# Kernel optimization log

Measured on AMD Instinct MI355X. Metric: run time of the kernel, lower is better.

Reference implementation:

```python
import jax, jax.numpy as jnp
import numpy as np

N_NODES = 50000
IN_DIM = 128
OUT_DIM = 128
N_EDGES = 800000


def setup_inputs() -> dict:
    key = jax.random.key(0)
    k1, k2, k3, k4 = jax.random.split(key, 4)
    h = jax.random.normal(k1, (N_NODES, IN_DIM), dtype=jnp.float32)
    edges = jax.random.randint(k2, (2, N_EDGES), 0, N_NODES, dtype=jnp.int64)
    # nn.Linear params
    lim = 1.0 / np.sqrt(IN_DIM)
    W = jax.random.uniform(k3, (OUT_DIM, IN_DIM), minval=-lim, maxval=lim, dtype=jnp.float32)
    b = jax.random.uniform(k4, (OUT_DIM,), minval=-lim, maxval=lim, dtype=jnp.float32)
    return {"h": h, "W": W, "b": b, "edges": edges}


def reference(h, W, b, edges):
    n = h.shape[0]
    # add self loops (use_self_loops=True)
    loops = jnp.arange(n, dtype=edges.dtype)
    src = jnp.concatenate([edges[0], loops])  # [E+N]
    dst = jnp.concatenate([edges[1], loops])  # [E+N]
    # linear transform
    h_ = h @ W.T + b  # [N, out_dim]
    # symmetric normalization: 1/sqrt(deg(src)*deg(dst)), degrees incl. self loops
    deg = jax.ops.segment_sum(jnp.ones_like(dst, dtype=h.dtype), dst, num_segments=n)
    ew = jax.lax.rsqrt(deg[src] * deg[dst])  # [E+N]
    # edge-weighted scatter-sum aggregation
    agg = jax.ops.segment_sum(h_[src] * ew[:, None], dst, num_segments=n)
    return agg
```

## Files before the change

kernel.cpp:

```cpp
#include <hip/hip_runtime.h>


#define IN_DIM 128
#define OUT_DIM 128
#define CAP 40
#define NB_A 256
#define NBIN 196
#define BINW 256
#define CAPA 44
#define OVB 8
#define OVCAP 4096

typedef short bf16x8 __attribute__((ext_vector_type(8)));
typedef float f32x4 __attribute__((ext_vector_type(4)));
typedef unsigned short us8 __attribute__((ext_vector_type(8)));
typedef unsigned short us4 __attribute__((ext_vector_type(4)));

__device__ __forceinline__ unsigned short f2bf(float f) {
    unsigned u = __float_as_uint(f);
    u += 0x7fffu + ((u >> 16) & 1u);
    return (unsigned short)(u >> 16);
}
__device__ __forceinline__ float bf2f(unsigned short s) {
    return __uint_as_float(((unsigned)s) << 16);
}
__device__ __forceinline__ void accw(float4& acc, ushort4 v, float wt) {
    acc.x += wt * bf2f(v.x);
    acc.y += wt * bf2f(v.y);
    acc.z += wt * bf2f(v.z);
    acc.w += wt * bf2f(v.w);
}
__device__ __forceinline__ bf16x8 load_a8(const float* h, int row, int k0, int n) {
    bf16x8 r;
    if (row < n) {
        const float4* p = (const float4*)(h + (size_t)row * 128 + k0);
        float4 f0 = p[0], f1 = p[1];
        r[0] = (short)f2bf(f0.x); r[1] = (short)f2bf(f0.y);
        r[2] = (short)f2bf(f0.z); r[3] = (short)f2bf(f0.w);
        r[4] = (short)f2bf(f1.x); r[5] = (short)f2bf(f1.y);
        r[6] = (short)f2bf(f1.z); r[7] = (short)f2bf(f1.w);
    } else {
        r = (bf16x8){0, 0, 0, 0, 0, 0, 0, 0};
    }
    return r;
}

__global__ __launch_bounds__(256) void k_gb(
        const float* __restrict__ h, const float* __restrict__ W,
        const float* __restrict__ b, unsigned short* __restrict__ hsb, int n,
        const int* __restrict__ ed, unsigned* __restrict__ gbuf,
        int* __restrict__ gcnt, int* __restrict__ aovb, int2* __restrict__ aov,
        int* __restrict__ ctrs, int E, int ngemm) {
    __shared__ __align__(16) unsigned short sB[128 * 136];
    __shared__ int ovc;
    __shared__ int2 ovl[OVB];
    const int tid = threadIdx.x;

    if ((int)blockIdx.x >= ngemm) {
        int blk = blockIdx.x - ngemm;
        if (blk == 0 && tid == 0) ctrs[0] = 0;
        int* bc = (int*)sB;
        for (int i = tid; i < NBIN; i += 256) bc[i] = 0;
        if (tid == 0) ovc = 0;
        __syncthreads();
        const int chunk = (E + NB_A - 1) / NB_A;
        const int e0 = blk * chunk, e1 = min(E, e0 + chunk);
        for (int e = e0 + tid; e < e1; e += 256) {
            int s = ed[e];
            int d = ed[E + e];
            int bin = d >> 8, dlo = d & 255;
            int r = atomicAdd(&bc[bin], 1);
            if (r < CAPA) {
                gbuf[((size_t)blk * NBIN + bin) * CAPA + r] =
                    (unsigned)s | ((unsigned)dlo << 16);
            } else {
                int k = atomicAdd(&ovc, 1);
                if (k < OVB) ovl[k] = make_int2(s, d);
            }
        }
        __syncthreads();
        for (int i = tid; i < NBIN; i += 256)
            gcnt[(size_t)blk * NBIN + i] = min(bc[i], CAPA);
        int nov = min(ovc, OVB);
        if (tid < nov) aov[blk * OVB + tid] = ovl[tid];
        if (tid == 0) aovb[blk] = nov;
        return;
    }

    const int lane = tid & 63;
    const int wv = tid >> 6;
    const int quad = lane >> 4;
    const int l16 = lane & 15;
    const int row0 = blockIdx.x * 128;

    {
        const float4* W4 = (const float4*)W;
        for (int t = tid; t < 128 * 32; t += 256) {
            float4 w = W4[t];
            ushort4 q;
            q.x = f2bf(w.x); q.y = f2bf(w.y); q.z = f2bf(w.z); q.w = f2bf(w.w);
            ((ushort4*)sB)[(t >> 5) * 34 + (t & 31)] = q;
        }
    }
    __syncthreads();

    f32x4 acc[2][8];
#pragma unroll
    for (int mt = 0; mt < 2; ++mt)
#pragma unroll
        for (int nt = 0; nt < 8; ++nt) acc[mt][nt] = (f32x4){0.f, 0.f, 0.f, 0.f};

    const int koff = quad * 8;
    const int ra0 = row0 + wv * 32 + l16;
    const int ra1 = ra0 + 16;
#pragma unroll
    for (int kc = 0; kc < 4; ++kc) {
        int kbase = kc * 32 + koff;
        bf16x8 a0 = load_a8(h, ra0, kbase, n);
        bf16x8 a1 = load_a8(h, ra1, kbase, n);
#pragma unroll
        for (int nt = 0; nt < 8; ++nt) {
            bf16x8 bb = *(const bf16x8*)(sB + (nt * 16 + l16) * 136 + kbase);
            acc[0][nt] = __builtin_amdgcn_mfma_f32_16x16x32_bf16(a0, bb, acc[0][nt], 0, 0, 0);
            acc[1][nt] = __builtin_amdgcn_mfma_f32_16x16x32_bf16(a1, bb, acc[1][nt], 0, 0, 0);
        }
    }

#pragma unroll
    for (int mt = 0; mt < 2; ++mt) {
#pragma unroll
        for (int r = 0; r < 4; ++r) {
            int row = row0 + wv * 32 + mt * 16 + quad * 4 + r;
            if (row >= n) continue;
#pragma unroll
            for (int nt = 0; nt < 8; ++nt) {
                int col = nt * 16 + l16;
                hsb[(size_t)row * 128 + col] = f2bf(acc[mt][nt][r] + b[col]);
            }
        }
    }
}

__global__ __launch_bounds__(256) void k_binB(const unsigned* __restrict__ gbuf,
                                              const int* __restrict__ gcnt,
                                              const int* __restrict__ aovb,
                                              const int2* __restrict__ aov,
                                              unsigned short* __restrict__ ell,
                                              int* __restrict__ cnt,
                                              float* __restrict__ rs,
                                              int2* __restrict__ ovf2,
                                              int* __restrict__ ovf2c, int n) {
    __shared__ int pfx[NB_A + 1];
    __shared__ int ws4[4];
    __shared__ int lcnt[BINW];
    __shared__ __align__(16) unsigned short ells[BINW * CAP];
    const int tid = threadIdx.x;
    const int bin = blockIdx.x;
    const int node0 = bin << 8;
    const int lane = tid & 63;
    const int wv = tid >> 6;

    lcnt[tid] = 0;
    int c = gcnt[(size_t)tid * NBIN + bin];
    int x = c;
#pragma unroll
    for (int d = 1; d < 64; d <<= 1) {
        int t = __shfl_up(x, d, 64);
        if (lane >= d) x += t;
    }
    if (lane == 63) ws4[wv] = x;
    __syncthreads();
    if (tid == 0) {
        int a = 0;
#pragma unroll
        for (int j = 0; j < 4; ++j) { int t = ws4[j]; ws4[j] = a; a += t; }
    }
    __syncthreads();
    pfx[tid + 1] = ws4[wv] + x;
    if (tid == 0) pfx[0] = 0;
    __syncthreads();
    const int total = pfx[NB_A];

    for (int base = 0; base < total; base += 256) {
        int idx = base + tid;
        if (idx < total) {
            int lo = 0, hi = NB_A;
            while (hi - lo > 1) {
                int mid = (lo + hi) >> 1;
                if (pfx[mid] <= idx) lo = mid; else hi = mid;
            }
            unsigned rec = gbuf[((size_t)lo * NBIN + bin) * CAPA + (idx - pfx[lo])];
            int src = rec & 0xffff;
            int dlo = rec >> 16;
            int r = atomicAdd(&lcnt[dlo], 1);
            if (r < CAP) {
                ells[dlo * CAP + r] = (unsigned short)src;
            } else {
                int k = atomicAdd(ovf2c, 1);
                if (k < OVCAP) ovf2[k] = make_int2(src, node0 + dlo);
            }
        }
    }
    {
        int cov = aovb[tid];
        for (int j = 0; j < cov; ++j) {
            int2 p = aov[tid * OVB + j];
            if ((p.y >> 8) == bin) {
                int dlo = p.y & 255;
                int r = atomicAdd(&lcnt[dlo], 1);
                if (r < CAP) {
                    ells[dlo * CAP + r] = (unsigned short)p.x;
                } else {
                    int k = atomicAdd(ovf2c, 1);
                    if (k < OVCAP) ovf2[k] = make_int2(p.x, node0 + dlo);
                }
            }
        }
    }
    __syncthreads();
    int node = node0 + tid;
    if (node < n) {
        cnt[node] = lcnt[tid];
        rs[node] = rsqrtf((float)(lcnt[tid] + 1));
    }
    const int4* sp = (const int4*)ells;
    int4* dp = (int4*)(ell + (size_t)node0 * CAP);
#pragma unroll
    for (int i = tid; i < BINW * CAP * 2 / 16; i += 256) dp[i] = sp[i];
}

__global__ __launch_bounds__(256) void k_agg(const int* __restrict__ cnt,
                                             const float* __restrict__ rs,
                                             const unsigned short* __restrict__ ell,
                                             const int2* __restrict__ ovf2,
                                             const int* __restrict__ ovf2c,
                                             const unsigned short* __restrict__ hsb,
                                             float* __restrict__ out, int n) {
    int node = blockIdx.x * 8 + (threadIdx.x >> 5);
    if (node >= n) return;
    int lane = threadIdx.x & 31;
    int deg = cnt[node];
    float rsn = rs[node];
    int m = min(deg, CAP);

    const ushort4* hp = (const ushort4*)hsb;
    ushort4 sv = hp[(size_t)node * 32 + lane];
    float4 acc;
    acc.x = rsn * bf2f(sv.x); acc.y = rsn * bf2f(sv.y);
    acc.z = rsn * bf2f(sv.z); acc.w = rsn * bf2f(sv.w);

    const unsigned short* row = ell + (size_t)node * CAP;
    int e = 0;
    for (; e + 8 <= m; e += 8) {
        us8 p = *(const us8*)(row + e);
        float w0 = rs[p[0]], w1 = rs[p[1]], w2 = rs[p[2]], w3 = rs[p[3]];
        float w4 = rs[p[4]], w5 = rs[p[5]], w6 = rs[p[6]], w7 = rs[p[7]];
        ushort4 v0 = hp[(size_t)p[0] * 32 + lane];
        ushort4 v1 = hp[(size_t)p[1] * 32 + lane];
        ushort4 v2 = hp[(size_t)p[2] * 32 + lane];
        ushort4 v3 = hp[(size_t)p[3] * 32 + lane];
        ushort4 v4 = hp[(size_t)p[4] * 32 + lane];
        ushort4 v5 = hp[(size_t)p[5] * 32 + lane];
        ushort4 v6 = hp[(size_t)p[6] * 32 + lane];
        ushort4 v7 = hp[(size_t)p[7] * 32 + lane];
        accw(acc, v0, w0); accw(acc, v1, w1); accw(acc, v2, w2); accw(acc, v3, w3);
        accw(acc, v4, w4); accw(acc, v5, w5); accw(acc, v6, w6); accw(acc, v7, w7);
    }
    if (e + 4 <= m) {
        us4 p = *(const us4*)(row + e);
        float w0 = rs[p[0]], w1 = rs[p[1]], w2 = rs[p[2]], w3 = rs[p[3]];
        ushort4 v0 = hp[(size_t)p[0] * 32 + lane];
        ushort4 v1 = hp[(size_t)p[1] * 32 + lane];
        ushort4 v2 = hp[(size_t)p[2] * 32 + lane];
        ushort4 v3 = hp[(size_t)p[3] * 32 + lane];
        accw(acc, v0, w0); accw(acc, v1, w1); accw(acc, v2, w2); accw(acc, v3, w3);
        e += 4;
    }
    for (; e < m; ++e) {
        int s = row[e];
        accw(acc, hp[(size_t)s * 32 + lane], rs[s]);
    }
    if (deg > CAP) {
        int novf = min(*ovf2c, OVCAP);
        for (int i = 0; i < novf; ++i) {
            int2 p = ovf2[i];
            if (p.y == node) {
                accw(acc, hp[(size_t)p.x * 32 + lane], rs[p.x]);
            }
        }
    }
    acc.x *= rsn; acc.y *= rsn; acc.z *= rsn; acc.w *= rsn;
    ((float4*)out)[(size_t)node * 32 + lane] = acc;
}

extern "C" void kernel_launch(void* const* d_in, const int* in_sizes, int n_in,
                              void* d_out, int out_size, void* d_ws, size_t ws_size,
                              hipStream_t stream) {
    const float* h = (const float*)d_in[0];
    const float* W = (const float*)d_in[1];
    const float* b = (const float*)d_in[2];
    const int* edges = (const int*)d_in[3];

    const int n = in_sizes[0] / IN_DIM;
    const int E = in_sizes[3] / 2;
    const int ngemm = (n + 127) / 128;
    const int nnode_pad = NBIN * BINW;

    size_t o = 0;
    auto carve = [&](size_t elems) {
        size_t cur = o;
        o += (elems + 511) & ~(size_t)511;
        return cur;
    };
    float* ws = (float*)d_ws;
    unsigned short* hsb = (unsigned short*)(ws + carve((size_t)n * 64));
    unsigned* gbuf = (unsigned*)(ws + carve((size_t)NB_A * NBIN * CAPA));
    int* gcnt = (int*)(ws + carve((size_t)NB_A * NBIN));
    int* aovb = (int*)(ws + carve(NB_A));
    int2* aov = (int2*)(ws + carve((size_t)NB_A * OVB * 2));
    int* cnt = (int*)(ws + carve(nnode_pad));
    float* rs = ws + carve(nnode_pad);
    unsigned short* ell = (unsigned short*)(ws + carve((size_t)nnode_pad * CAP / 2));
    int2* ovf2 = (int2*)(ws + carve(OVCAP * 2));
    int* ctrs = (int*)(ws + carve(2));

    float* out = (float*)d_out;

    k_gb<<<ngemm + NB_A, 256, 0, stream>>>(h, W, b, hsb, n, edges, gbuf, gcnt,
                                           aovb, aov, ctrs, E, ngemm);
    k_binB<<<NBIN, 256, 0, stream>>>(gbuf, gcnt, aovb, aov, ell, cnt, rs,
                                     ovf2, ctrs, n);
    k_agg<<<(n + 7) / 8, 256, 0, stream>>>(cnt, rs, ell, ovf2, ctrs, hsb, out, n);
}
```

Baseline: 143.5 us.

## Use finer destination bins and 16-lane 16-byte gathers in aggregation

Destination bins shrink from 256 to 64 nodes, giving 784 bins with a 16-record capacity per producer block. This lets each thread in the bin kernel scan one producer cell directly, replacing the block prefix scan and the per-record binary search. The aggregation kernel now gives each node 16 lanes that each load 8 bf16 values at once, so every gathered row is fetched with wider loads and each block covers twice as many nodes. The cost is more bin blocks, uneven per-thread serial loops in the bin kernel, and more register pressure in aggregation from the 8-float accumulators.

Result: no change. 142.6 us (-0.6%).

```diff
diff --git a/kernel.cpp b/kernel.cpp
--- a/kernel.cpp
+++ b/kernel.cpp
@@ -5,9 +5,9 @@
 #define OUT_DIM 128
 #define CAP 40
 #define NB_A 256
-#define NBIN 196
-#define BINW 256
-#define CAPA 44
+#define NBIN 784
+#define BINW 64
+#define CAPA 16
 #define OVB 8
 #define OVCAP 4096
 
@@ -23,12 +23,6 @@
 }
 __device__ __forceinline__ float bf2f(unsigned short s) {
     return __uint_as_float(((unsigned)s) << 16);
-}
-__device__ __forceinline__ void accw(float4& acc, ushort4 v, float wt) {
-    acc.x += wt * bf2f(v.x);
-    acc.y += wt * bf2f(v.y);
-    acc.z += wt * bf2f(v.z);
-    acc.w += wt * bf2f(v.w);
 }
 __device__ __forceinline__ bf16x8 load_a8(const float* h, int row, int k0, int n) {
     bf16x8 r;
@@ -68,7 +62,7 @@
         for (int e = e0 + tid; e < e1; e += 256) {
             int s = ed[e];
             int d = ed[E + e];
-            int bin = d >> 8, dlo = d & 255;
+            int bin = d >> 6, dlo = d & 63;
             int r = atomicAdd(&bc[bin], 1);
             if (r < CAPA) {
                 gbuf[((size_t)blk * NBIN + bin) * CAPA + r] =
@@ -150,46 +144,20 @@
                                               float* __restrict__ rs,
                                               int2* __restrict__ ovf2,
                                               int* __restrict__ ovf2c, int n) {
-    __shared__ int pfx[NB_A + 1];
-    __shared__ int ws4[4];
     __shared__ int lcnt[BINW];
     __shared__ __align__(16) unsigned short ells[BINW * CAP];
     const int tid = threadIdx.x;
     const int bin = blockIdx.x;
-    const int node0 = bin << 8;
-    const int lane = tid & 63;
-    const int wv = tid >> 6;
-
-    lcnt[tid] = 0;
-    int c = gcnt[(size_t)tid * NBIN + bin];
-    int x = c;
-#pragma unroll
-    for (int d = 1; d < 64; d <<= 1) {
-        int t = __shfl_up(x, d, 64);
-        if (lane >= d) x += t;
-    }
-    if (lane == 63) ws4[wv] = x;
+    const int node0 = bin * BINW;
+
+    if (tid < BINW) lcnt[tid] = 0;
     __syncthreads();
-    if (tid == 0) {
-        int a = 0;
-#pragma unroll
-        for (int j = 0; j < 4; ++j) { int t = ws4[j]; ws4[j] = a; a += t; }
-    }
-    __syncthreads();
-    pfx[tid + 1] = ws4[wv] + x;
-    if (tid == 0) pfx[0] = 0;
-    __syncthreads();
-    const int total = pfx[NB_A];
-
-    for (int base = 0; base < total; base += 256) {
-        int idx = base + tid;
-        if (idx < total) {
-            int lo = 0, hi = NB_A;
-            while (hi - lo > 1) {
-                int mid = (lo + hi) >> 1;
-                if (pfx[mid] <= idx) lo = mid; else hi = mid;
-            }
-            unsigned rec = gbuf[((size_t)lo * NBIN + bin) * CAPA + (idx - pfx[lo])];
+
+    {
+        int c = gcnt[(size_t)tid * NBIN + bin];
+        const unsigned* cell = gbuf + ((size_t)tid * NBIN + bin) * CAPA;
+        for (int j = 0; j < c; ++j) {
+            unsigned rec = cell[j];
             int src = rec & 0xffff;
             int dlo = rec >> 16;
             int r = atomicAdd(&lcnt[dlo], 1);
@@ -205,8 +173,8 @@
         int cov = aovb[tid];
         for (int j = 0; j < cov; ++j) {
             int2 p = aov[tid * OVB + j];
-            if ((p.y >> 8) == bin) {
-                int dlo = p.y & 255;
+            if ((p.y >> 6) == bin) {
+                int dlo = p.y & 63;
                 int r = atomicAdd(&lcnt[dlo], 1);
                 if (r < CAP) {
                     ells[dlo * CAP + r] = (unsigned short)p.x;
@@ -218,10 +186,12 @@
         }
     }
     __syncthreads();
-    int node = node0 + tid;
-    if (node < n) {
-        cnt[node] = lcnt[tid];
-        rs[node] = rsqrtf((float)(lcnt[tid] + 1));
+    if (tid < BINW) {
+        int node = node0 + tid;
+        if (node < n) {
+            cnt[node] = lcnt[tid];
+            rs[node] = rsqrtf((float)(lcnt[tid] + 1));
+        }
     }
     const int4* sp = (const int4*)ells;
     int4* dp = (int4*)(ell + (size_t)node0 * CAP);
@@ -236,18 +206,18 @@
                                              const int* __restrict__ ovf2c,
                                              const unsigned short* __restrict__ hsb,
                                              float* __restrict__ out, int n) {
-    int node = blockIdx.x * 8 + (threadIdx.x >> 5);
+    int node = blockIdx.x * 16 + (threadIdx.x >> 4);
     if (node >= n) return;
-    int lane = threadIdx.x & 31;
+    int lane = threadIdx.x & 15;
     int deg = cnt[node];
     float rsn = rs[node];
     int m = min(deg, CAP);
 
-    const ushort4* hp = (const ushort4*)hsb;
-    ushort4 sv = hp[(size_t)node * 32 + lane];
-    float4 acc;
-    acc.x = rsn * bf2f(sv.x); acc.y = rsn * bf2f(sv.y);
-    acc.z = rsn * bf2f(sv.z); acc.w = rsn * bf2f(sv.w);
+    const us8* hp = (const us8*)hsb;
+    us8 sv = hp[(size_t)node * 16 + lane];
+    float acc[8];
+#pragma unroll
+    for (int k = 0; k < 8; ++k) acc[k] = rsn * bf2f((unsigned short)sv[k]);
 
     const unsigned short* row = ell + (size_t)node * CAP;
     int e = 0;
@@ -255,42 +225,66 @@
         us8 p = *(const us8*)(row + e);
         float w0 = rs[p[0]], w1 = rs[p[1]], w2 = rs[p[2]], w3 = rs[p[3]];
         float w4 = rs[p[4]], w5 = rs[p[5]], w6 = rs[p[6]], w7 = rs[p[7]];
-        ushort4 v0 = hp[(size_t)p[0] * 32 + lane];
-        ushort4 v1 = hp[(size_t)p[1] * 32 + lane];
-        ushort4 v2 = hp[(size_t)p[2] * 32 + lane];
-        ushort4 v3 = hp[(size_t)p[3] * 32 + lane];
-        ushort4 v4 = hp[(size_t)p[4] * 32 + lane];
-        ushort4 v5 = hp[(size_t)p[5] * 32 + lane];
-        ushort4 v6 = hp[(size_t)p[6] * 32 + lane];
-        ushort4 v7 = hp[(size_t)p[7] * 32 + lane];
-        accw(acc, v0, w0); accw(acc, v1, w1); accw(acc, v2, w2); accw(acc, v3, w3);
-        accw(acc, v4, w4); accw(acc, v5, w5); accw(acc, v6, w6); accw(acc, v7, w7);
+        us8 v0 = hp[(size_t)p[0] * 16 + lane];
+        us8 v1 = hp[(size_t)p[1] * 16 + lane];
+        us8 v2 = hp[(size_t)p[2] * 16 + lane];
+        us8 v3 = hp[(size_t)p[3] * 16 + lane];
+        us8 v4 = hp[(size_t)p[4] * 16 + lane];
+        us8 v5 = hp[(size_t)p[5] * 16 + lane];
+        us8 v6 = hp[(size_t)p[6] * 16 + lane];
+        us8 v7 = hp[(size_t)p[7] * 16 + lane];
+#pragma unroll
+        for (int k = 0; k < 8; ++k) {
+            acc[k] += w0 * bf2f((unsigned short)v0[k]);
+            acc[k] += w1 * bf2f((unsigned short)v1[k]);
+            acc[k] += w2 * bf2f((unsigned short)v2[k]);
+            acc[k] += w3 * bf2f((unsigned short)v3[k]);
+            acc[k] += w4 * bf2f((unsigned short)v4[k]);
+            acc[k] += w5 * bf2f((unsigned short)v5[k]);
+            acc[k] += w6 * bf2f((unsigned short)v6[k]);
+            acc[k] += w7 * bf2f((unsigned short)v7[k]);
+        }
     }
     if (e + 4 <= m) {
         us4 p = *(const us4*)(row + e);
         float w0 = rs[p[0]], w1 = rs[p[1]], w2 = rs[p[2]], w3 = rs[p[3]];
-        ushort4 v0 = hp[(size_t)p[0] * 32 + lane];
-        ushort4 v1 = hp[(size_t)p[1] * 32 + lane];
-        ushort4 v2 = hp[(size_t)p[2] * 32 + lane];
-        ushort4 v3 = hp[(size_t)p[3] * 32 + lane];
-        accw(acc, v0, w0); accw(acc, v1, w1); accw(acc, v2, w2); accw(acc, v3, w3);
+        us8 v0 = hp[(size_t)p[0] * 16 + lane];
+        us8 v1 = hp[(size_t)p[1] * 16 + lane];
+        us8 v2 = hp[(size_t)p[2] * 16 + lane];
+        us8 v3 = hp[(size_t)p[3] * 16 + lane];
+#pragma unroll
+        for (int k = 0; k < 8; ++k) {
+            acc[k] += w0 * bf2f((unsigned short)v0[k]);
+            acc[k] += w1 * bf2f((unsigned short)v1[k]);
+            acc[k] += w2 * bf2f((unsigned short)v2[k]);
+            acc[k] += w3 * bf2f((unsigned short)v3[k]);
+        }
         e += 4;
     }
     for (; e < m; ++e) {
         int s = row[e];
-        accw(acc, hp[(size_t)s * 32 + lane], rs[s]);
+        float wt = rs[s];
+        us8 v = hp[(size_t)s * 16 + lane];
+#pragma unroll
+        for (int k = 0; k < 8; ++k) acc[k] += wt * bf2f((unsigned short)v[k]);
     }
     if (deg > CAP) {
         int novf = min(*ovf2c, OVCAP);
         for (int i = 0; i < novf; ++i) {
             int2 p = ovf2[i];
             if (p.y == node) {
-                accw(acc, hp[(size_t)p.x * 32 + lane], rs[p.x]);
-            }
-        }
-    }
-    acc.x *= rsn; acc.y *= rsn; acc.z *= rsn; acc.w *= rsn;
-    ((float4*)out)[(size_t)node * 32 + lane] = acc;
+                float wt = rs[p.x];
+                us8 v = hp[(size_t)p.x * 16 + lane];
+#pragma unroll
+                for (int k = 0; k < 8; ++k) acc[k] += wt * bf2f((unsigned short)v[k]);
+            }
+        }
+    }
+    float4 o0 = make_float4(rsn * acc[0], rsn * acc[1], rsn * acc[2], rsn * acc[3]);
+    float4 o1 = make_float4(rsn * acc[4], rsn * acc[5], rsn * acc[6], rsn * acc[7]);
+    float* op = out + (size_t)node * 128 + lane * 8;
+    *(float4*)op = o0;
+    *(float4*)(op + 4) = o1;
 }
 
 extern "C" void kernel_launch(void* const* d_in, const int* in_sizes, int n_in,
@@ -330,5 +324,5 @@
                                            aovb, aov, ctrs, E, ngemm);
     k_binB<<<NBIN, 256, 0, stream>>>(gbuf, gcnt, aovb, aov, ell, cnt, rs,
                                      ovf2, ctrs, n);
-    k_agg<<<(n + 7) / 8, 256, 0, stream>>>(cnt, rs, ell, ovf2, ctrs, hsb, out, n);
-}
+    k_agg<<<(n + 15) / 16, 256, 0, stream>>>(cnt, rs, ell, ovf2, ctrs, hsb, out, n);
+}
```

## Use finer 64-node destination bins and per-thread cell walks in binning

Applied to the files above, without the earlier changes.

Destination bins shrink from 256 to 64 nodes, so there are 784 bins with a per-block cell capacity of 16. The second binning kernel now launches four times as many blocks. Each thread walks its own source-block cell instead of the block building a prefix scan and doing a binary search. This removes the scan, the extra syncs and the search, and gives more parallelism in the second pass. The cost is more serial per-thread loops, more bin counters and gcnt entries, and a higher chance of overflow with the smaller CAPA of 16.

Measured after the change: 140.4 us. 1.02x faster.

```diff
diff --git a/kernel.cpp b/kernel.cpp
--- a/kernel.cpp
+++ b/kernel.cpp
@@ -5,9 +5,9 @@
 #define OUT_DIM 128
 #define CAP 40
 #define NB_A 256
-#define NBIN 196
-#define BINW 256
-#define CAPA 44
+#define NBIN 784
+#define BINW 64
+#define CAPA 16
 #define OVB 8
 #define OVCAP 4096
 
@@ -68,7 +68,7 @@
         for (int e = e0 + tid; e < e1; e += 256) {
             int s = ed[e];
             int d = ed[E + e];
-            int bin = d >> 8, dlo = d & 255;
+            int bin = d >> 6, dlo = d & 63;
             int r = atomicAdd(&bc[bin], 1);
             if (r < CAPA) {
                 gbuf[((size_t)blk * NBIN + bin) * CAPA + r] =
@@ -150,46 +150,20 @@
                                               float* __restrict__ rs,
                                               int2* __restrict__ ovf2,
                                               int* __restrict__ ovf2c, int n) {
-    __shared__ int pfx[NB_A + 1];
-    __shared__ int ws4[4];
     __shared__ int lcnt[BINW];
     __shared__ __align__(16) unsigned short ells[BINW * CAP];
     const int tid = threadIdx.x;
     const int bin = blockIdx.x;
-    const int node0 = bin << 8;
-    const int lane = tid & 63;
-    const int wv = tid >> 6;
-
-    lcnt[tid] = 0;
-    int c = gcnt[(size_t)tid * NBIN + bin];
-    int x = c;
-#pragma unroll
-    for (int d = 1; d < 64; d <<= 1) {
-        int t = __shfl_up(x, d, 64);
-        if (lane >= d) x += t;
-    }
-    if (lane == 63) ws4[wv] = x;
+    const int node0 = bin * BINW;
+
+    if (tid < BINW) lcnt[tid] = 0;
     __syncthreads();
-    if (tid == 0) {
-        int a = 0;
-#pragma unroll
-        for (int j = 0; j < 4; ++j) { int t = ws4[j]; ws4[j] = a; a += t; }
-    }
-    __syncthreads();
-    pfx[tid + 1] = ws4[wv] + x;
-    if (tid == 0) pfx[0] = 0;
-    __syncthreads();
-    const int total = pfx[NB_A];
-
-    for (int base = 0; base < total; base += 256) {
-        int idx = base + tid;
-        if (idx < total) {
-            int lo = 0, hi = NB_A;
-            while (hi - lo > 1) {
-                int mid = (lo + hi) >> 1;
-                if (pfx[mid] <= idx) lo = mid; else hi = mid;
-            }
-            unsigned rec = gbuf[((size_t)lo * NBIN + bin) * CAPA + (idx - pfx[lo])];
+
+    {
+        int c = gcnt[(size_t)tid * NBIN + bin];
+        const unsigned* cell = gbuf + ((size_t)tid * NBIN + bin) * CAPA;
+        for (int j = 0; j < c; ++j) {
+            unsigned rec = cell[j];
             int src = rec & 0xffff;
             int dlo = rec >> 16;
             int r = atomicAdd(&lcnt[dlo], 1);
@@ -205,8 +179,8 @@
         int cov = aovb[tid];
         for (int j = 0; j < cov; ++j) {
             int2 p = aov[tid * OVB + j];
-            if ((p.y >> 8) == bin) {
-                int dlo = p.y & 255;
+            if ((p.y >> 6) == bin) {
+                int dlo = p.y & 63;
                 int r = atomicAdd(&lcnt[dlo], 1);
                 if (r < CAP) {
                     ells[dlo * CAP + r] = (unsigned short)p.x;
@@ -218,10 +192,12 @@
         }
     }
     __syncthreads();
-    int node = node0 + tid;
-    if (node < n) {
-        cnt[node] = lcnt[tid];
-        rs[node] = rsqrtf((float)(lcnt[tid] + 1));
+    if (tid < BINW) {
+        int node = node0 + tid;
+        if (node < n) {
+            cnt[node] = lcnt[tid];
+            rs[node] = rsqrtf((float)(lcnt[tid] + 1));
+        }
     }
     const int4* sp = (const int4*)ells;
     int4* dp = (int4*)(ell + (size_t)node0 * CAP);
```
